# Optimization experiments

Measured on AMD Instinct MI355X. Metric: run time of the kernel, lower is better.

## Reference

```python
import jax, jax.numpy as jnp
import numpy as np

B, S, D, H, F = 2, 2048, 1024, 16, 4096
DK = D // H
EPS = 1e-6


def _ln(x, g, b):
    mu = jnp.mean(x, axis=-1, keepdims=True)
    var = jnp.mean(jnp.square(x - mu), axis=-1, keepdims=True)
    return (x - mu) * jax.lax.rsqrt(var + EPS) * g + b


def setup_inputs() -> dict:
    key = jax.random.key(0)
    ks = jax.random.split(key, 8)
    sc = 0.02
    return {
        "x": jax.random.normal(ks[0], (B, S, D), jnp.float32),
        "wq": jax.random.normal(ks[1], (D, D), jnp.float32) * sc,
        "bq": jnp.zeros((D,), jnp.float32),
        "wk": jax.random.normal(ks[2], (D, D), jnp.float32) * sc,
        "bk": jnp.zeros((D,), jnp.float32),
        "wv": jax.random.normal(ks[3], (D, D), jnp.float32) * sc,
        "bv": jnp.zeros((D,), jnp.float32),
        "wo": jax.random.normal(ks[4], (D, D), jnp.float32) * sc,
        "bo": jnp.zeros((D,), jnp.float32),
        "w1": jax.random.normal(ks[5], (D, F), jnp.float32) * sc,
        "b1": jnp.zeros((F,), jnp.float32),
        "w2": jax.random.normal(ks[6], (F, D), jnp.float32) * sc,
        "b2": jnp.zeros((D,), jnp.float32),
        "g1": jnp.ones((D,), jnp.float32),
        "be1": jnp.zeros((D,), jnp.float32),
        "g2": jnp.ones((D,), jnp.float32),
        "be2": jnp.zeros((D,), jnp.float32),
    }


def reference(x, wq, bq, wk, bk, wv, bv, wo, bo, w1, b1, w2, b2, g1, be1, g2, be2):
    # Multi-head self-attention (no masks, eval-mode dropout = identity)
    q = (x @ wq + bq).reshape(B, S, H, DK)
    k = (x @ wk + bk).reshape(B, S, H, DK)
    v = (x @ wv + bv).reshape(B, S, H, DK)
    scale = 1.0 / (DK ** 0.5)
    score = jnp.einsum('bihd,bjhd->bhij', q, k) * scale  # [B,H,S,S]
    p = jax.nn.softmax(score, axis=-1)
    attn = jnp.einsum('bhij,bjhd->bihd', p, v).reshape(B, S, D)
    attn = attn @ wo + bo
    # residual + LayerNorm 1
    h = _ln(x + attn, g1, be1)
    # FFN (relu) + residual + LayerNorm 2
    ff = jax.nn.relu(h @ w1 + b1) @ w2 + b2
    return _ln(h + ff, g2, be2)
```

## Files before the change

kernel.cpp:

```cpp
#include <hip/hip_runtime.h>
#include <hip/hip_bf16.h>
#include <cmath>

typedef __bf16 bf16_t;
typedef __bf16 bf16x4 __attribute__((ext_vector_type(4)));
typedef __bf16 bf16x8 __attribute__((ext_vector_type(8)));
typedef float  f32x4  __attribute__((ext_vector_type(4)));

__device__ __forceinline__ void gld_lds16(const bf16_t* g, bf16_t* l) {
    __builtin_amdgcn_global_load_lds(
        (const __attribute__((address_space(1))) void*)g,
        (__attribute__((address_space(3))) void*)l,
        16, 0, 0);
}


struct PrepArgs {
    const float* w[6]; bf16_t* wt[6];
    int K[6], N[6], start[6];
    const float* x; bf16_t* xb; int castStart;
    const float* bq; const float* bk; float* bqkv; int biasStart;
};

__global__ __launch_bounds__(256) void prep(PrepArgs pa) {
    __shared__ float tile[32][33];
    const int bid = blockIdx.x, t = threadIdx.x;
    if (bid < pa.castStart) {
        int mi = 0;
#pragma unroll
        for (int i = 1; i < 6; i++) if (bid >= pa.start[i]) mi = i;
        const int tt  = bid - pa.start[mi];
        const int nbx = pa.N[mi] >> 5;
        const int n0 = (tt % nbx) * 32, k0 = (tt / nbx) * 32;
        const float* in = pa.w[mi];
        bf16_t* out = pa.wt[mi];
        const int K = pa.K[mi], N = pa.N[mi];
        const int tx = t & 31, ty = t >> 5;
#pragma unroll
        for (int i = 0; i < 4; i++) {
            int kk = ty + i * 8;
            tile[kk][tx] = in[(size_t)(k0 + kk) * N + n0 + tx];
        }
        __syncthreads();
#pragma unroll
        for (int i = 0; i < 4; i++) {
            int nn = ty + i * 8;
            out[(size_t)(n0 + nn) * K + k0 + tx] = (bf16_t)tile[tx][nn];
        }
    } else if (bid < pa.biasStart) {
        int i = (bid - pa.castStart) * 256 + t;
        f32x4 v = ((const f32x4*)pa.x)[i];
        bf16x4 o;
        o[0] = (bf16_t)v[0]; o[1] = (bf16_t)v[1]; o[2] = (bf16_t)v[2]; o[3] = (bf16_t)v[3];
        ((bf16x4*)pa.xb)[i] = o;
    } else {
#pragma unroll
        for (int j = 0; j < 8; j++) {
            int idx = t * 8 + j;
            pa.bqkv[idx] = idx < 1024 ? pa.bq[idx] : pa.bk[idx - 1024];
        }
    }
}

template<int BN>
__global__ __launch_bounds__(512, 1) void gemm_deep(
    const bf16_t* __restrict__ A, const bf16_t* __restrict__ Bt,
    const float* __restrict__ bias, bf16_t* __restrict__ Cb,
    int M, int N, int lda, int Kloc, int relu, int nbn) {
    constexpr int NT = BN / 64;
    constexpr int WN = BN / 4;
    __shared__ __attribute__((aligned(16))) bf16_t As[4][256 * 32];
    __shared__ __attribute__((aligned(16))) bf16_t Bs[4][BN * 32];
    const int tid  = threadIdx.x;
    const int lane = tid & 63;
    const int wave = tid >> 6;
    const int wm = wave >> 2, wn = wave & 3;
    const int kh = blockIdx.z;

    const int span  = 8 * nbn;
    const int group = blockIdx.x / span;
    const int rem   = blockIdx.x % span;
    const int bm    = group * 8 + (rem & 7);
    const int bn    = rem >> 3;

    bf16_t* Cb_b = Cb + (size_t)kh * M * N;
    const int koff = kh * Kloc;

    const int srow   = tid >> 2;
    const int slot_s = ((tid & 3) ^ ((tid >> 3) & 3)) * 8;
    const bf16_t* Ag = A  + (size_t)(bm * 256 + srow) * lda + koff + slot_s;
    const bf16_t* Bg = Bt + (size_t)(bn * BN  + srow) * lda + koff + slot_s;

    auto stage = [&](int kk, int buf) {
        gld_lds16(Ag + kk,                       &As[buf][0]        + tid * 8);
        gld_lds16(Ag + (size_t)128 * lda + kk,   &As[buf][128 * 32] + tid * 8);
        gld_lds16(Bg + kk,                       &Bs[buf][0]        + tid * 8);
        if constexpr (BN == 256)
            gld_lds16(Bg + (size_t)128 * lda + kk, &Bs[buf][128 * 32] + tid * 8);
    };

    f32x4 acc[8][NT] = {};
    const int mrow = lane & 15;
    const int qsw  = (((lane >> 4) ^ ((mrow >> 1) & 3))) * 8;

    auto compute = [&](int cur) {
        bf16x8 bfr[NT], af[8];
#pragma unroll
        for (int n = 0; n < NT; n++)
            bfr[n] = *(const bf16x8*)(&Bs[cur][(wn * WN + n * 16 + mrow) * 32 + qsw]);
#pragma unroll
        for (int mt = 0; mt < 8; mt++)
            af[mt] = *(const bf16x8*)(&As[cur][(wm * 128 + mt * 16 + mrow) * 32 + qsw]);
        __builtin_amdgcn_s_setprio(1);
#pragma unroll
        for (int mt = 0; mt < 8; mt++)
#pragma unroll
            for (int n = 0; n < NT; n++)
                acc[mt][n] = __builtin_amdgcn_mfma_f32_16x16x32_bf16(
                    af[mt], bfr[n], acc[mt][n], 0, 0, 0);
        __builtin_amdgcn_s_setprio(0);
    };

    stage(0, 0); stage(32, 1); stage(64, 2);
    const int nst = Kloc >> 5;
    for (int t = 0; t + 3 < nst; ++t) {
        stage((t + 3) * 32, (t + 3) & 3);
        if constexpr (BN == 256) asm volatile("s_waitcnt vmcnt(12)" ::: "memory");
        else                     asm volatile("s_waitcnt vmcnt(9)"  ::: "memory");
        __builtin_amdgcn_s_barrier();
        compute(t & 3);
        asm volatile("s_waitcnt lgkmcnt(0)" ::: "memory");
        __builtin_amdgcn_s_barrier();
    }
    if constexpr (BN == 256) asm volatile("s_waitcnt vmcnt(8)" ::: "memory");
    else                     asm volatile("s_waitcnt vmcnt(6)" ::: "memory");
    __builtin_amdgcn_s_barrier();
    compute((nst - 3) & 3);
    asm volatile("s_waitcnt lgkmcnt(0)" ::: "memory");
    __builtin_amdgcn_s_barrier();
    if constexpr (BN == 256) asm volatile("s_waitcnt vmcnt(4)" ::: "memory");
    else                     asm volatile("s_waitcnt vmcnt(3)" ::: "memory");
    __builtin_amdgcn_s_barrier();
    compute((nst - 2) & 3);
    asm volatile("s_waitcnt lgkmcnt(0)" ::: "memory");
    __builtin_amdgcn_s_barrier();
    asm volatile("s_waitcnt vmcnt(0)" ::: "memory");
    __builtin_amdgcn_s_barrier();
    compute((nst - 1) & 3);

    const int rq = (lane >> 4) * 4;
#pragma unroll
    for (int mt = 0; mt < 8; mt++) {
        int row0 = bm * 256 + wm * 128 + mt * 16 + rq;
#pragma unroll
        for (int n = 0; n < NT; n++) {
            int col = bn * BN + wn * WN + n * 16 + mrow;
            float bvc = (bias && kh == 0) ? bias[col] : 0.f;
#pragma unroll
            for (int r = 0; r < 4; r++) {
                float v = acc[mt][n][r] + bvc;
                if (relu) v = fmaxf(v, 0.f);
                Cb_b[(size_t)(row0 + r) * N + col] = (bf16_t)v;
            }
        }
    }
}

template<int BM, int BN>
__global__ __launch_bounds__(512, 2) void gemm_tile(
    const bf16_t* __restrict__ A, const bf16_t* __restrict__ Bt,
    const float* __restrict__ bias,
    float* __restrict__ Cf, bf16_t* __restrict__ Cb,
    int M, int N, int lda, int Kloc, int relu, int nbn) {
    constexpr int MF = BM / 32;
    constexpr int NT = BN / 64;
    constexpr int WM = BM / 2;
    constexpr int WN = BN / 4;
    __shared__ __attribute__((aligned(16))) bf16_t As[2][2][BM * 32];
    __shared__ __attribute__((aligned(16))) bf16_t Bs[2][2][BN * 32];
    const int tid  = threadIdx.x;
    const int lane = tid & 63;
    const int wave = tid >> 6;
    const int wm = wave >> 2, wn = wave & 3;
    const int kh = blockIdx.z;

    const int span  = 8 * nbn;
    const int group = blockIdx.x / span;
    const int rem   = blockIdx.x % span;
    const int bm    = group * 8 + (rem & 7);
    const int bn    = rem >> 3;

    float*  Cf_b = Cf ? Cf + (size_t)kh * M * N : nullptr;
    const int koff = kh * Kloc;

    const int r4 = tid >> 2;
    const int kcs = ((tid & 3) ^ ((tid >> 3) & 3)) * 8;
    const bf16_t* Ag = A  + (size_t)(bm * BM + r4) * lda + koff + kcs;
    const bf16_t* Bg = Bt + (size_t)(bn * BN + r4) * lda + koff + kcs;

    f32x4 acc[MF][NT] = {};
    const int mrow = lane & 15;
    const int qsw  = (((lane >> 4) ^ ((mrow >> 1) & 3))) * 8;

    auto stage = [&](int kk, int buf) {
#pragma unroll
        for (int hh = 0; hh < 2; hh++) {
#pragma unroll
            for (int i = 0; i < BM / 128; i++)
                gld_lds16(Ag + (size_t)(i * 128) * lda + kk + hh * 32,
                          &As[buf][hh][i * 128 * 32] + tid * 8);
#pragma unroll
            for (int i = 0; i < BN / 128; i++)
                gld_lds16(Bg + (size_t)(i * 128) * lda + kk + hh * 32,
                          &Bs[buf][hh][i * 128 * 32] + tid * 8);
        }
    };

    stage(0, 0);
    __syncthreads();

    const int nsteps = Kloc >> 6;
    for (int st = 0; st < nsteps; ++st) {
        const int cur = st & 1;
        if (st + 1 < nsteps) stage((st + 1) << 6, cur ^ 1);

#pragma unroll
        for (int hh = 0; hh < 2; hh++) {
            bf16x8 bfr[NT];
#pragma unroll
            for (int n = 0; n < NT; n++)
                bfr[n] = *(const bf16x8*)(&Bs[cur][hh][(wn * WN + n * 16 + mrow) * 32 + qsw]);
            __builtin_amdgcn_s_setprio(1);
#pragma unroll
            for (int mt = 0; mt < MF; mt++) {
                bf16x8 af = *(const bf16x8*)(&As[cur][hh][(wm * WM + mt * 16 + mrow) * 32 + qsw]);
#pragma unroll
                for (int n = 0; n < NT; n++)
                    acc[mt][n] = __builtin_amdgcn_mfma_f32_16x16x32_bf16(
                        af, bfr[n], acc[mt][n], 0, 0, 0);
            }
            __builtin_amdgcn_s_setprio(0);
        }
        __syncthreads();
    }

    const int rq = (lane >> 4) * 4;
#pragma unroll
    for (int mt = 0; mt < MF; mt++) {
        int row0 = bm * BM + wm * WM + mt * 16 + rq;
#pragma unroll
        for (int n = 0; n < NT; n++) {
            int col = bn * BN + wn * WN + n * 16 + mrow;
            float bvc = (bias && kh == 0) ? bias[col] : 0.f;
#pragma unroll
            for (int r = 0; r < 4; r++) {
                float v = acc[mt][n][r] + bvc;
                if (relu) v = fmaxf(v, 0.f);
                size_t idx = (size_t)(row0 + r) * N + col;
                if (Cf_b) Cf_b[idx] = v;
                if (Cb)   Cb[idx]   = (bf16_t)v;
            }
        }
    }
}

template<int MT>
__global__ __launch_bounds__(256) void gemm_bt(
    const bf16_t* __restrict__ A, const bf16_t* __restrict__ Bt,
    const float* __restrict__ bias,
    float* __restrict__ Cf, bf16_t* __restrict__ Cb,
    int M, int N, int lda, int Kloc, int relu, int nbn, int bias_row,
    long bt_bstride, long c_bstride) {
    constexpr int TM = MT * 32;
    __shared__ __attribute__((aligned(16))) bf16_t As[2][TM * 32];
    __shared__ __attribute__((aligned(16))) bf16_t Bs[2][128 * 32];
    const int tid  = threadIdx.x;
    const int lane = tid & 63;
    const int wave = tid >> 6;
    const int wm = wave & 1, wn = wave >> 1;
    const int kh = blockIdx.z;

    const int span  = 8 * nbn;
    const int group = blockIdx.x / span;
    const int rem   = blockIdx.x % span;
    const int bm    = group * 8 + (rem & 7);
    const int bn    = rem >> 3;

    const bf16_t* Bt_b = Bt + (size_t)blockIdx.y * bt_bstride;
    float*  Cf_b = Cf ? Cf + (size_t)blockIdx.y * c_bstride + (size_t)kh * M * N : nullptr;
    bf16_t* Cb_b = Cb ? Cb + (size_t)blockIdx.y * c_bstride : nullptr;
    const int koff = kh * Kloc;

    const int r4 = tid >> 2;
    const int kcs = ((tid & 3) ^ ((tid >> 3) & 3)) * 8;
    const bf16_t* Ag = A    + (size_t)(bm * TM  + r4) * lda + koff + kcs;
    const bf16_t* Bg = Bt_b + (size_t)(bn * 128 + r4) * lda + koff + kcs;

    f32x4 acc[MT][4] = {};
    const int mrow = lane & 15;
    const int qsw  = (((lane >> 4) ^ ((mrow >> 1) & 3))) * 8;

    auto stage = [&](int kk, int buf) {
#pragma unroll
        for (int i = 0; i < MT / 2; i++)
            gld_lds16(Ag + (size_t)(i * 64) * lda + kk, &As[buf][i * 64 * 32] + tid * 8);
        gld_lds16(Bg + kk,                        &Bs[buf][0] + tid * 8);
        gld_lds16(Bg + (size_t)64 * lda + kk,     &Bs[buf][64 * 32] + tid * 8);
    };

    stage(0, 0);
    __syncthreads();

    const int nt = Kloc >> 5;
    for (int t7 = 0; t7 < nt; ++t7) {
        const int cur = t7 & 1;
        if (t7 + 1 < nt) stage((t7 + 1) << 5, cur ^ 1);

        bf16x8 af[MT], bfr[4];
#pragma unroll
        for (int mt = 0; mt < MT; mt++)
            af[mt] = *(const bf16x8*)(&As[cur][(wm * (MT * 16) + mt * 16 + mrow) * 32 + qsw]);
#pragma unroll
        for (int nt2 = 0; nt2 < 4; nt2++)
            bfr[nt2] = *(const bf16x8*)(&Bs[cur][(wn * 64 + nt2 * 16 + mrow) * 32 + qsw]);
#pragma unroll
        for (int mt = 0; mt < MT; mt++)
#pragma unroll
            for (int nt2 = 0; nt2 < 4; nt2++)
                acc[mt][nt2] = __builtin_amdgcn_mfma_f32_16x16x32_bf16(
                    af[mt], bfr[nt2], acc[mt][nt2], 0, 0, 0);

        __syncthreads();
    }

    const int rq = (lane >> 4) * 4;
#pragma unroll
    for (int mt = 0; mt < MT; mt++) {
        int row0 = bm * TM + wm * (MT * 16) + mt * 16 + rq;
#pragma unroll
        for (int nt2 = 0; nt2 < 4; nt2++) {
            int col = bn * 128 + wn * 64 + nt2 * 16 + mrow;
            float bvc = (bias && kh == 0 && !bias_row) ? bias[col] : 0.f;
#pragma unroll
            for (int r = 0; r < 4; r++) {
                float bb = (bias && kh == 0 && bias_row) ? bias[row0 + r] : bvc;
                float v = acc[mt][nt2][r] + bb;
                if (relu) v = fmaxf(v, 0.f);
                size_t idx = (size_t)(row0 + r) * N + col;
                if (Cf_b) Cf_b[idx] = v;
                if (Cb_b) Cb_b[idx] = (bf16_t)v;
            }
        }
    }
}

__global__ __launch_bounds__(512) void flash_attn_mfma(
    const bf16_t* __restrict__ QKb,
    const bf16_t* __restrict__ Vtg,
    bf16_t* __restrict__ Outb) {
    __shared__ __attribute__((aligned(16))) bf16_t Ks[2][4096];
    __shared__ __attribute__((aligned(16))) bf16_t Vs[2][4096];
    __shared__ __attribute__((aligned(16))) bf16_t Ps[8192];
    const int t = threadIdx.x;
    const int lane = t & 63, wave = t >> 6;
    const int g = lane >> 4, cl = lane & 15;
    const int b = blockIdx.z, h = blockIdx.y, q0 = blockIdx.x * 128;
    const int RS = 2048;
    const bf16_t* Qg = QKb + (size_t)(b * 2048 + q0) * RS + h * 64;
    const bf16_t* Kg = QKb + (size_t)(b * 2048) * RS + 1024 + h * 64;
    const bf16_t* Vg = Vtg + ((size_t)b * 1024 + h * 64) * 2048;

    const int sr   = (t >> 2) & 63;
    const int half = t >> 8;
    const int scs  = half * 32 + (((t & 3) ^ ((t >> 3) & 3)) * 8);

    const float C = 0.125f * 1.4426950408889634f;
    const bf16_t* Qrow = Qg + (size_t)(wave * 16 + cl) * RS;
    bf16x8 qr0 = *(const bf16x8*)(Qrow + g * 8);
    bf16x8 qr1 = *(const bf16x8*)(Qrow + 32 + g * 8);
#pragma unroll
    for (int j = 0; j < 8; j++) {
        qr0[j] = (bf16_t)((float)qr0[j] * C);
        qr1[j] = (bf16_t)((float)qr1[j] * C);
    }

    const bf16_t* Kst = Kg + (size_t)sr * RS + scs;
    const bf16_t* Vst = Vg + (size_t)sr * 2048 + scs;

    gld_lds16(Kst, &Ks[0][0] + t * 8);
    gld_lds16(Vst, &Vs[0][0] + t * 8);
    __syncthreads();

    f32x4 Oacc[4] = {};
    f32x4 Lacc = {};
    bf16x8 ones;
#pragma unroll
    for (int j = 0; j < 8; j++) ones[j] = (bf16_t)1.0f;

    const int rowb = wave * 16 + cl;
    const int psw  = (cl & 7) << 4;
    const int gsw  = ((g ^ ((cl >> 1) & 3))) * 8;
    char* PsB = (char*)Ps;

    for (int kt_i = 0; kt_i < 32; ++kt_i) {
        const int cur = kt_i & 1;
        if (kt_i + 1 < 32) {
            Kst += (size_t)64 * RS;
            Vst += 64;
            gld_lds16(Kst, &Ks[cur ^ 1][0] + t * 8);
            gld_lds16(Vst, &Vs[cur ^ 1][0] + t * 8);
        }

        f32x4 Sacc[4] = {};
        __builtin_amdgcn_s_setprio(1);
#pragma unroll
        for (int ks = 0; ks < 2; ++ks) {
            bf16x8 bq = ks ? qr1 : qr0;
#pragma unroll
            for (int mt = 0; mt < 4; ++mt) {
                bf16x8 ak = *(const bf16x8*)(&Ks[cur][ks * 2048 + (mt * 16 + cl) * 32 + gsw]);
                Sacc[mt] = __builtin_amdgcn_mfma_f32_16x16x32_bf16(ak, bq, Sacc[mt], 0, 0, 0);
            }
        }
        __builtin_amdgcn_s_setprio(0);

#pragma unroll
        for (int mt = 0; mt < 4; ++mt) {
            bf16x4 p4;
#pragma unroll
            for (int r = 0; r < 4; r++)
                p4[r] = (bf16_t)__builtin_amdgcn_exp2f(Sacc[mt][r]);
            *(bf16x4*)(PsB + ((rowb * 128 + mt * 32 + g * 8) ^ psw)) = p4;
        }

        __builtin_amdgcn_s_setprio(1);
#pragma unroll
        for (int ks = 0; ks < 2; ++ks) {
            bf16x8 ap = *(const bf16x8*)(PsB + ((rowb * 128 + ks * 64 + g * 16) ^ psw));
            Lacc = __builtin_amdgcn_mfma_f32_16x16x32_bf16(ap, ones, Lacc, 0, 0, 0);
#pragma unroll
            for (int nt = 0; nt < 4; ++nt) {
                bf16x8 bv = *(const bf16x8*)(&Vs[cur][ks * 2048 + (nt * 16 + cl) * 32 + gsw]);
                Oacc[nt] = __builtin_amdgcn_mfma_f32_16x16x32_bf16(ap, bv, Oacc[nt], 0, 0, 0);
            }
        }
        __builtin_amdgcn_s_setprio(0);

        __syncthreads();
    }

#pragma unroll
    for (int r = 0; r < 4; r++) {
        float inv = 1.f / Lacc[r];
        int qrow = q0 + wave * 16 + g * 4 + r;
        size_t base = (size_t)(b * 2048 + qrow) * 1024 + h * 64;
#pragma unroll
        for (int nt = 0; nt < 4; nt++)
            Outb[base + nt * 16 + cl] = (bf16_t)(Oacc[nt][r] * inv);
    }
}

__global__ __launch_bounds__(256) void resid_ln4(const float* __restrict__ a,
                                                 const bf16_t* __restrict__ p,
                                                 long pstr,
                                                 const float* __restrict__ g,
                                                 const float* __restrict__ be,
                                                 float* __restrict__ outf,
                                                 bf16_t* __restrict__ outb) {
    const int row = blockIdx.x, t = threadIdx.x;
    const size_t base = (size_t)row * 1024;
    f32x4 v = ((const f32x4*)(a + base))[t];
#pragma unroll
    for (int j = 0; j < 4; j++) {
        bf16x4 pv = ((const bf16x4*)(p + (size_t)j * pstr + base))[t];
        v[0] += (float)pv[0]; v[1] += (float)pv[1];
        v[2] += (float)pv[2]; v[3] += (float)pv[3];
    }
    float sum = v[0] + v[1] + v[2] + v[3];
    float sq  = v[0] * v[0] + v[1] * v[1] + v[2] * v[2] + v[3] * v[3];
#pragma unroll
    for (int o = 1; o < 64; o <<= 1) {
        sum += __shfl_xor(sum, o);
        sq  += __shfl_xor(sq, o);
    }
    __shared__ float red[8];
    int wave = t >> 6, lane = t & 63;
    if (lane == 0) { red[wave] = sum; red[4 + wave] = sq; }
    __syncthreads();
    sum = red[0] + red[1] + red[2] + red[3];
    sq  = red[4] + red[5] + red[6] + red[7];
    float mu  = sum * (1.f / 1024.f);
    float var = sq * (1.f / 1024.f) - mu * mu;
    float rs  = rsqrtf(var + 1e-6f);
    f32x4 g4 = ((const f32x4*)g)[t];
    f32x4 b4 = ((const f32x4*)be)[t];
    f32x4 o = (v - mu) * rs * g4 + b4;
    ((f32x4*)(outf + base))[t] = o;
    if (outb) {
        bf16x4 ob;
        ob[0] = (bf16_t)o[0]; ob[1] = (bf16_t)o[1]; ob[2] = (bf16_t)o[2]; ob[3] = (bf16_t)o[3];
        ((bf16x4*)(outb + base))[t] = ob;
    }
}

extern "C" void kernel_launch(void* const* d_in, const int* in_sizes, int n_in,
                              void* d_out, int out_size, void* d_ws, size_t ws_size,
                              hipStream_t stream) {
    (void)in_sizes; (void)n_in; (void)out_size; (void)ws_size;
    const float* x   = (const float*)d_in[0];
    const float* wq  = (const float*)d_in[1];
    const float* bq  = (const float*)d_in[2];
    const float* wk  = (const float*)d_in[3];
    const float* bk  = (const float*)d_in[4];
    const float* wv  = (const float*)d_in[5];
    const float* bv  = (const float*)d_in[6];
    const float* wo  = (const float*)d_in[7];
    const float* bo  = (const float*)d_in[8];
    const float* w1  = (const float*)d_in[9];
    const float* b1  = (const float*)d_in[10];
    const float* w2  = (const float*)d_in[11];
    const float* b2  = (const float*)d_in[12];
    const float* g1  = (const float*)d_in[13];
    const float* be1 = (const float*)d_in[14];
    const float* g2  = (const float*)d_in[15];
    const float* be2 = (const float*)d_in[16];
    float* out = (float*)d_out;

    char* ws = (char*)d_ws;
    const size_t MB = 1ull << 20;
    bf16_t* xb    = (bf16_t*)(ws + 0);
    bf16_t* WtQKV = (bf16_t*)(ws + 8 * MB);
    bf16_t* WtO   = (bf16_t*)(ws + 14 * MB);
    bf16_t* Wt1   = (bf16_t*)(ws + 16 * MB);
    bf16_t* Wt2   = (bf16_t*)(ws + 24 * MB);
    float*  bqkv  = (float*)(ws + 32 * MB);
    bf16_t* QKb   = (bf16_t*)(ws + 33 * MB);
    bf16_t* Vt    = (bf16_t*)(ws + 49 * MB);
    bf16_t* ffb   = (bf16_t*)(ws + 33 * MB);
    bf16_t* oab   = (bf16_t*)(ws + 65 * MB);
    bf16_t* f2b   = (bf16_t*)(ws + 65 * MB);
    float*  hbuf  = (float*)(ws + 97 * MB);
    bf16_t* hb    = (bf16_t*)(ws + 113 * MB);
    bf16_t* ab    = xb;
    const long MN = 4096 * 1024;

    PrepArgs pa;
    pa.w[0] = wq; pa.w[1] = wk; pa.w[2] = wv; pa.w[3] = wo; pa.w[4] = w1; pa.w[5] = w2;
    pa.wt[0] = WtQKV; pa.wt[1] = WtQKV + 1024 * 1024; pa.wt[2] = WtQKV + 2048 * 1024;
    pa.wt[3] = WtO; pa.wt[4] = Wt1; pa.wt[5] = Wt2;
    int Ks[6] = {1024, 1024, 1024, 1024, 1024, 4096};
    int Ns[6] = {1024, 1024, 1024, 1024, 4096, 1024};
    int st[6] = {0, 1024, 2048, 3072, 4096, 8192};
    for (int i = 0; i < 6; i++) { pa.K[i] = Ks[i]; pa.N[i] = Ns[i]; pa.start[i] = st[i]; }
    pa.x = x; pa.xb = xb; pa.castStart = 12288;
    pa.bq = bq; pa.bk = bk; pa.bqkv = bqkv; pa.biasStart = 12288 + 4096;
    prep<<<12288 + 4096 + 1, 256, 0, stream>>>(pa);

    gemm_tile<128, 256><<<256, 512, 0, stream>>>(xb, WtQKV, bqkv, nullptr, QKb,
                                        4096, 2048, 1024, 1024, 0, 8);
    gemm_bt<2><<<dim3(256, 2, 1), 256, 0, stream>>>(WtQKV + 2048 * 1024, xb, bv,
                                        nullptr, Vt, 1024, 2048, 1024, 1024, 0, 16, 1,
                                        (long)2048 * 1024, (long)1024 * 2048);
    flash_attn_mfma<<<dim3(16, 16, 2), 512, 0, stream>>>(QKb, Vt, ab);
    gemm_deep<256><<<dim3(64, 1, 4), 512, 0, stream>>>(ab, WtO, bo, oab,
                                        4096, 1024, 1024, 256, 0, 4);
    resid_ln4<<<4096, 256, 0, stream>>>(x, oab, MN, g1, be1, hbuf, hb);
    gemm_deep<256><<<256, 512, 0, stream>>>(hb, Wt1, b1, ffb,
                                        4096, 4096, 1024, 1024, 1, 16);
    gemm_deep<256><<<dim3(64, 1, 4), 512, 0, stream>>>(ffb, Wt2, b2, f2b,
                                        4096, 1024, 4096, 1024, 0, 4);
    resid_ln4<<<4096, 256, 0, stream>>>(hbuf, f2b, MN, g2, be2, out, nullptr);
}
```

Measured before the change: 372.2 us.

## Remap workgroups across XCDs and switch FFN2 to 2-way split-K tile GEMM

Adds an XCD-aware remapping of workgroup IDs in gemm_deep, gemm_tile and the flash attention kernel, so that consecutive logical tiles land on the same chiplet and share its L2. FFN2 moves from gemm_deep with a 4-way K split to gemm_tile<128,256> with a 2-way split and bf16 partial outputs, and resid_ln4 now sums a runtime number of partials. The aim is better cache locality and less partial-sum traffic, at the cost of different occupancy and tile shape for the FFN2 GEMM and a non-unrolled reduction loop.

```diff
diff --git a/kernel.cpp b/kernel.cpp
--- a/kernel.cpp
+++ b/kernel.cpp
@@ -75,11 +75,17 @@
     const int lane = tid & 63;
     const int wave = tid >> 6;
     const int wm = wave >> 2, wn = wave & 3;
-    const int kh = blockIdx.z;
+
+    const int nwgx = gridDim.x;
+    const int flat = blockIdx.x + nwgx * blockIdx.z;
+    const int nwg  = nwgx * gridDim.z;
+    const int logical = (flat & 7) * (nwg >> 3) + (flat >> 3);
+    const int lx = logical % nwgx;
+    const int kh = logical / nwgx;
 
     const int span  = 8 * nbn;
-    const int group = blockIdx.x / span;
-    const int rem   = blockIdx.x % span;
+    const int group = lx / span;
+    const int rem   = lx % span;
     const int bm    = group * 8 + (rem & 7);
     const int bn    = rem >> 3;
 
@@ -169,8 +175,7 @@
 template<int BM, int BN>
 __global__ __launch_bounds__(512, 2) void gemm_tile(
     const bf16_t* __restrict__ A, const bf16_t* __restrict__ Bt,
-    const float* __restrict__ bias,
-    float* __restrict__ Cf, bf16_t* __restrict__ Cb,
+    const float* __restrict__ bias, bf16_t* __restrict__ Cb,
     int M, int N, int lda, int Kloc, int relu, int nbn) {
     constexpr int MF = BM / 32;
     constexpr int NT = BN / 64;
@@ -182,15 +187,21 @@
     const int lane = tid & 63;
     const int wave = tid >> 6;
     const int wm = wave >> 2, wn = wave & 3;
-    const int kh = blockIdx.z;
+
+    const int nwgx = gridDim.x;
+    const int flat = blockIdx.x + nwgx * blockIdx.z;
+    const int nwg  = nwgx * gridDim.z;
+    const int logical = (flat & 7) * (nwg >> 3) + (flat >> 3);
+    const int lx = logical % nwgx;
+    const int kh = logical / nwgx;
 
     const int span  = 8 * nbn;
-    const int group = blockIdx.x / span;
-    const int rem   = blockIdx.x % span;
+    const int group = lx / span;
+    const int rem   = lx % span;
     const int bm    = group * 8 + (rem & 7);
     const int bn    = rem >> 3;
 
-    float*  Cf_b = Cf ? Cf + (size_t)kh * M * N : nullptr;
+    bf16_t* Cb_b = Cb + (size_t)kh * M * N;
     const int koff = kh * Kloc;
 
     const int r4 = tid >> 2;
@@ -256,9 +267,7 @@
             for (int r = 0; r < 4; r++) {
                 float v = acc[mt][n][r] + bvc;
                 if (relu) v = fmaxf(v, 0.f);
-                size_t idx = (size_t)(row0 + r) * N + col;
-                if (Cf_b) Cf_b[idx] = v;
-                if (Cb)   Cb[idx]   = (bf16_t)v;
+                Cb_b[(size_t)(row0 + r) * N + col] = (bf16_t)v;
             }
         }
     }
@@ -364,7 +373,13 @@
     const int t = threadIdx.x;
     const int lane = t & 63, wave = t >> 6;
     const int g = lane >> 4, cl = lane & 15;
-    const int b = blockIdx.z, h = blockIdx.y, q0 = blockIdx.x * 128;
+
+    const int flat = blockIdx.x + 16 * blockIdx.y + 256 * blockIdx.z;
+    const int logical = (flat & 7) * 64 + (flat >> 3);
+    const int q0 = (logical & 15) * 128;
+    const int h  = (logical >> 4) & 15;
+    const int b  = logical >> 8;
+
     const int RS = 2048;
     const bf16_t* Qg = QKb + (size_t)(b * 2048 + q0) * RS + h * 64;
     const bf16_t* Kg = QKb + (size_t)(b * 2048) * RS + 1024 + h * 64;
@@ -462,7 +477,7 @@
 
 __global__ __launch_bounds__(256) void resid_ln4(const float* __restrict__ a,
                                                  const bf16_t* __restrict__ p,
-                                                 long pstr,
+                                                 long pstr, int np,
                                                  const float* __restrict__ g,
                                                  const float* __restrict__ be,
                                                  float* __restrict__ outf,
@@ -470,8 +485,7 @@
     const int row = blockIdx.x, t = threadIdx.x;
     const size_t base = (size_t)row * 1024;
     f32x4 v = ((const f32x4*)(a + base))[t];
-#pragma unroll
-    for (int j = 0; j < 4; j++) {
+    for (int j = 0; j < np; j++) {
         bf16x4 pv = ((const bf16x4*)(p + (size_t)j * pstr + base))[t];
         v[0] += (float)pv[0]; v[1] += (float)pv[1];
         v[2] += (float)pv[2]; v[3] += (float)pv[3];
@@ -556,7 +570,7 @@
     pa.bq = bq; pa.bk = bk; pa.bqkv = bqkv; pa.biasStart = 12288 + 4096;
     prep<<<12288 + 4096 + 1, 256, 0, stream>>>(pa);
 
-    gemm_tile<128, 256><<<256, 512, 0, stream>>>(xb, WtQKV, bqkv, nullptr, QKb,
+    gemm_tile<128, 256><<<256, 512, 0, stream>>>(xb, WtQKV, bqkv, QKb,
                                         4096, 2048, 1024, 1024, 0, 8);
     gemm_bt<2><<<dim3(256, 2, 1), 256, 0, stream>>>(WtQKV + 2048 * 1024, xb, bv,
                                         nullptr, Vt, 1024, 2048, 1024, 1024, 0, 16, 1,
@@ -564,10 +578,10 @@
     flash_attn_mfma<<<dim3(16, 16, 2), 512, 0, stream>>>(QKb, Vt, ab);
     gemm_deep<256><<<dim3(64, 1, 4), 512, 0, stream>>>(ab, WtO, bo, oab,
                                         4096, 1024, 1024, 256, 0, 4);
-    resid_ln4<<<4096, 256, 0, stream>>>(x, oab, MN, g1, be1, hbuf, hb);
+    resid_ln4<<<4096, 256, 0, stream>>>(x, oab, MN, 4, g1, be1, hbuf, hb);
     gemm_deep<256><<<256, 512, 0, stream>>>(hb, Wt1, b1, ffb,
                                         4096, 4096, 1024, 1024, 1, 16);
-    gemm_deep<256><<<dim3(64, 1, 4), 512, 0, stream>>>(ffb, Wt2, b2, f2b,
-                                        4096, 1024, 4096, 1024, 0, 4);
-    resid_ln4<<<4096, 256, 0, stream>>>(hbuf, f2b, MN, g2, be2, out, nullptr);
-}
+    gemm_tile<128, 256><<<dim3(128, 1, 2), 512, 0, stream>>>(ffb, Wt2, b2, f2b,
+                                        4096, 1024, 4096, 2048, 0, 4);
+    resid_ln4<<<4096, 256, 0, stream>>>(hbuf, f2b, MN, 2, g2, be2, out, nullptr);
+}
```

Result: no change. 371.4 us (-0.2%).
